# Optimization experiments

Hardware: AMD Instinct MI355X
Metric: run time of the kernel (lower is better)

Reference implementation:

```python
import jax, jax.numpy as jnp
import numpy as np

B, S, H = 2, 2048, 2048
NH, NKV, HD = 16, 4, 128
NEG = -1e9


def rotate_half(x):
    x1, x2 = x[..., : x.shape[-1] // 2], x[..., x.shape[-1] // 2 :]
    return jnp.concatenate((-x2, x1), axis=-1)


def setup_inputs() -> dict:
    key = jax.random.key(0)
    ks = jax.random.split(key, 6)
    hidden_states = jax.random.normal(ks[0], (B, S, H), dtype=jnp.float32)
    # causal additive mask [B, 1, S, S]
    causal = jnp.tril(jnp.ones((S, S), dtype=bool))
    attention_mask = jnp.where(causal, 0.0, NEG).astype(jnp.float32)
    attention_mask = jnp.broadcast_to(attention_mask, (B, 1, S, S))
    # rotary embeddings, base 10000
    inv_freq = 1.0 / (10000.0 ** (np.arange(0, HD, 2, dtype=np.float32) / HD))
    pos = np.arange(S, dtype=np.float32)
    freqs = np.outer(pos, inv_freq)  # [S, HD/2]
    emb = np.concatenate([freqs, freqs], axis=-1)  # [S, HD]
    cos = jnp.broadcast_to(jnp.asarray(np.cos(emb)), (B, S, HD))
    sin = jnp.broadcast_to(jnp.asarray(np.sin(emb)), (B, S, HD))
    sc = 0.02
    Wq = jax.random.normal(ks[1], (H, NH * HD), dtype=jnp.float32) * sc
    Wk = jax.random.normal(ks[2], (H, NKV * HD), dtype=jnp.float32) * sc
    Wv = jax.random.normal(ks[3], (H, NKV * HD), dtype=jnp.float32) * sc
    Wo = jax.random.normal(ks[4], (H, H), dtype=jnp.float32) * sc
    return {"hidden_states": hidden_states, "attention_mask": attention_mask,
            "cos": cos, "sin": sin, "Wq": Wq, "Wk": Wk, "Wv": Wv, "Wo": Wo}


def reference(hidden_states, attention_mask, cos, sin, Wq, Wk, Wv, Wo):
    b, s, _ = hidden_states.shape
    # projections -> [b, heads, s, hd]
    q = (hidden_states @ Wq).reshape(b, s, NH, HD).transpose(0, 2, 1, 3)
    k = (hidden_states @ Wk).reshape(b, s, NKV, HD).transpose(0, 2, 1, 3)
    v = (hidden_states @ Wv).reshape(b, s, NKV, HD).transpose(0, 2, 1, 3)
    # RoPE (cos/sin unsqueezed at dim 1)
    c, sn = cos[:, None], sin[:, None]
    q = q * c + rotate_half(q) * sn
    k = k * c + rotate_half(k) * sn
    # GQA repeat_kv: [b, nkv, s, hd] -> [b, nh, s, hd]
    n_rep = NH // NKV
    k = jnp.repeat(k, n_rep, axis=1)
    v = jnp.repeat(v, n_rep, axis=1)
    scores = jnp.einsum("bhqd,bhkd->bhqk", q, k) / jnp.sqrt(jnp.float32(HD))
    scores = scores + attention_mask
    probs = jax.nn.softmax(scores.astype(jnp.float32), axis=-1).astype(q.dtype)
    out = jnp.einsum("bhqk,bhkd->bhqd", probs, v)
    out = out.transpose(0, 2, 1, 3).reshape(b, s, NH * HD)
    return out @ Wo
```

## Files before the change

kernel.cpp:

```cpp
#include <hip/hip_runtime.h>
#include <hip/hip_bf16.h>

typedef __bf16 bf16;
typedef __bf16 bf16x4 __attribute__((ext_vector_type(4)));
typedef __bf16 bf16x8 __attribute__((ext_vector_type(8)));
typedef float f32x4 __attribute__((ext_vector_type(4)));

__device__ __forceinline__ void gload_lds16(const void* g, void* l) {
  __builtin_amdgcn_global_load_lds((__attribute__((address_space(1))) void*)(g),
                                   (__attribute__((address_space(3))) void*)(l), 16, 0, 0);
}
__device__ __forceinline__ float fexp2(float x) {
  float r;
  asm volatile("v_exp_f32 %0, %1" : "=v"(r) : "v"(x));
  return r;
}
#define S_WAITCNT_VM(n) asm volatile("s_waitcnt vmcnt(" #n ")" ::: "memory")
#define LDS_FENCE() asm volatile("" ::: "memory")

__global__ void k_diag(float* __restrict__ o, float v) { o[threadIdx.x] = v; }

__global__ void k_cvt_bf16(const float* __restrict__ x, bf16* __restrict__ y, int n4) {
  int i = blockIdx.x * blockDim.x + threadIdx.x;
  if (i < n4) {
    float4 v = reinterpret_cast<const float4*>(x)[i];
    bf16x4 o = {(bf16)v.x, (bf16)v.y, (bf16)v.z, (bf16)v.w};
    reinterpret_cast<bf16x4*>(y)[i] = o;
  }
}

__global__ void k_transpose_w(const float* __restrict__ W, bf16* __restrict__ Wt, int K, int N) {
  __shared__ float tile[32][33];
  int kb = blockIdx.x * 32, nb = blockIdx.y * 32;
  int tx = threadIdx.x & 31, ty = threadIdx.x >> 5;
#pragma unroll
  for (int i = 0; i < 32; i += 8)
    tile[ty + i][tx] = W[(size_t)(kb + ty + i) * N + nb + tx];
  __syncthreads();
#pragma unroll
  for (int i = 0; i < 32; i += 8)
    Wt[(size_t)(nb + ty + i) * K + kb + tx] = (bf16)tile[tx][ty + i];
}

__global__ void k_transpose_v(const bf16* __restrict__ Cq, bf16* __restrict__ Vt) {
  __shared__ bf16 tile[32][34];
  constexpr int S = 2048, CSTR = 3072;
  int sb = blockIdx.x * 32, db = blockIdx.y * 32, bh = blockIdx.z;
  int b = bh >> 2, kvh = bh & 3;
  int tx = threadIdx.x & 31, ty = threadIdx.x >> 5;
  const bf16* src = Cq + (size_t)b * S * CSTR + 2560 + kvh * 128;
#pragma unroll
  for (int i = 0; i < 32; i += 8)
    tile[ty + i][tx] = src[(size_t)(sb + ty + i) * CSTR + db + tx];
  __syncthreads();
  bf16* dst = Vt + (size_t)bh * 128 * S;
#pragma unroll
  for (int i = 0; i < 32; i += 8)
    dst[(size_t)(db + ty + i) * S + sb + tx] = tile[tx][ty + i];
}

template <typename OT>
__global__ __launch_bounds__(512) void k_gemm4(const bf16* __restrict__ A,
                                               const bf16* __restrict__ B0,
                                               const bf16* __restrict__ B1, int nsplit,
                                               OT* __restrict__ C, int Ncols, int Kd) {
  __shared__ __align__(16) char lds[131072];
  const int t = threadIdx.x, w = t >> 6, l = t & 63;
  const int lr = l & 15, lk = l >> 4;
  const int gx = gridDim.x;
  const int flat = blockIdx.y * gx + blockIdx.x;
  const int xcd = flat & 7, local = flat >> 3;
  const int mi = (xcd & 3) * (gx >> 2) + (local & ((gx >> 2) - 1));
  const int ni = (xcd >> 2) * (gridDim.y >> 1) + (local >> 2);
  const int m0 = mi * 256, n0 = ni * 256;
  const int wm = w >> 2, wn = w & 3;
  const bf16* Bt = (n0 < nsplit) ? B0 + (size_t)n0 * Kd : B1 + (size_t)(n0 - nsplit) * Kd;
  const int nkt = Kd >> 6;
  const int srow8 = l >> 3;
  const int sk = ((l & 7) ^ srow8) * 8;
  auto stA = [&](int kt, int g) {
    if (kt >= nkt) return;
    const bf16* s = A + (size_t)(m0 + w * 32 + g * 8 + srow8) * Kd + (kt << 6) + sk;
    gload_lds16(s, lds + (kt & 1) * 32768 + (w * 32 + g * 8) * 128);
  };
  auto stB = [&](int kt, int g) {
    if (kt >= nkt) return;
    const bf16* s = Bt + (size_t)(w * 32 + g * 8 + srow8) * Kd + (kt << 6) + sk;
    gload_lds16(s, lds + 65536 + (kt & 1) * 32768 + (w * 32 + g * 8) * 128);
  };

  f32x4 acc[8][4] = {};
#pragma unroll
  for (int g = 0; g < 4; ++g) { stA(0, g); stB(0, g); }

  for (int kt = 0; kt < nkt; ++kt) {
    const char* Ab = lds + (kt & 1) * 32768;
    const char* Bb = lds + 65536 + (kt & 1) * 32768;
    bf16x8 bfr[4];
#pragma unroll
    for (int kk = 0; kk < 2; ++kk) {
#pragma unroll
      for (int h = 0; h < 2; ++h) {
        if (kk == 0 && h == 0) { S_WAITCNT_VM(0); }
        __builtin_amdgcn_s_barrier();
        LDS_FENCE();
        const int ph = kk * 2 + h;
        stA(kt + 1, ph);
        stB(kt + 1, ph);
        const int rc = ((kk * 4 + lk) ^ (lr & 7)) << 4;
        bf16x8 af[4];
#pragma unroll
        for (int i = 0; i < 4; ++i)
          af[i] = *reinterpret_cast<const bf16x8*>(Ab + (wm * 128 + (h * 4 + i) * 16 + lr) * 128 + rc);
        if (h == 0) {
#pragma unroll
          for (int j = 0; j < 4; ++j)
            bfr[j] = *reinterpret_cast<const bf16x8*>(Bb + (wn * 64 + j * 16 + lr) * 128 + rc);
        }
        __builtin_amdgcn_s_setprio(1);
#pragma unroll
        for (int i = 0; i < 4; ++i)
#pragma unroll
          for (int j = 0; j < 4; ++j)
            acc[h * 4 + i][j] = __builtin_amdgcn_mfma_f32_16x16x32_bf16(af[i], bfr[j], acc[h * 4 + i][j], 0, 0, 0);
        __builtin_amdgcn_s_setprio(0);
      }
    }
  }
#pragma unroll
  for (int i = 0; i < 8; ++i)
#pragma unroll
    for (int j = 0; j < 4; ++j)
#pragma unroll
      for (int r = 0; r < 4; ++r) {
        int row = m0 + wm * 128 + i * 16 + lk * 4 + r;
        int col = n0 + wn * 64 + j * 16 + lr;
        if constexpr (sizeof(OT) == 4)
          C[(size_t)row * Ncols + col] = acc[i][j][r];
        else
          C[(size_t)row * Ncols + col] = (bf16)acc[i][j][r];
      }
}

template <int BM, typename OT>
__global__ __launch_bounds__(512) void k_gemm2(const bf16* __restrict__ A, const bf16* __restrict__ Bt,
                                               OT* __restrict__ C, int N, int Kd) {
  constexpr int NA = (BM / 16) * 2;
  constexpr int NB = 16;
  constexpr int NST = NA + NB;
  constexpr int NSW = NST / 8;
  constexpr int WM = BM / 4;
  constexpr int RG = WM / 16;
  __shared__ __align__(16) bf16 sAB[2][NST * 512];
  const int t = threadIdx.x, w = t >> 6, l = t & 63;
  const int lr = l & 15, lk = l >> 4;
  const int gx = gridDim.x;
  const int nwg = gx * gridDim.y;
  const int flat = blockIdx.y * gx + blockIdx.x;
  const int vid = (flat & 7) * (nwg >> 3) + (flat >> 3);
  const int m0 = (vid % gx) * BM, n0 = (vid / gx) * 128;
  const int wm = w >> 1, wn = w & 1;
  const int srow = l >> 2;
  const int lchunk = (l & 3) ^ (((l >> 5) & 1) << 1);
  const int rdoff = lr * 64 + ((lk * 16) ^ ((lr >> 3) << 5));
  const int nkt = Kd >> 6;
  char* lds = (char*)sAB;

  auto stage = [&](int kt, int buf) {
    const int k0 = kt << 6;
#pragma unroll
    for (int u = 0; u < NSW; ++u) {
      const int s = w * NSW + u;
      const bf16* src;
      if (s < NA)
        src = A + (size_t)(m0 + (s >> 1) * 16 + srow) * Kd + k0 + (s & 1) * 32 + lchunk * 8;
      else
        src = Bt + (size_t)(n0 + ((s - NA) >> 1) * 16 + srow) * Kd + k0 + ((s - NA) & 1) * 32 + lchunk * 8;
      gload_lds16(src, lds + buf * (NST * 1024) + s * 1024);
    }
  };

  f32x4 acc[RG][4] = {};
  stage(0, 0);
  stage(1, 1);
  if constexpr (NSW == 6) S_WAITCNT_VM(6); else S_WAITCNT_VM(4);
  __builtin_amdgcn_s_barrier();
  int c = 0;
  for (int kt = 0; kt < nkt; ++kt) {
    __builtin_amdgcn_sched_barrier(0);
    const char* base = lds + c * (NST * 1024);
    bf16x8 af[RG][2], bfr[4][2];
#pragma unroll
    for (int i = 0; i < RG; ++i)
#pragma unroll
      for (int kk = 0; kk < 2; ++kk)
        af[i][kk] = *reinterpret_cast<const bf16x8*>(base + ((wm * RG + i) * 2 + kk) * 1024 + rdoff);
#pragma unroll
    for (int j = 0; j < 4; ++j)
#pragma unroll
      for (int kk = 0; kk < 2; ++kk)
        bfr[j][kk] = *reinterpret_cast<const bf16x8*>(base + (NA + (wn * 4 + j) * 2 + kk) * 1024 + rdoff);
    __builtin_amdgcn_s_setprio(1);
#pragma unroll
    for (int i = 0; i < RG; ++i)
#pragma unroll
      for (int j = 0; j < 4; ++j) {
        acc[i][j] = __builtin_amdgcn_mfma_f32_16x16x32_bf16(af[i][0], bfr[j][0], acc[i][j], 0, 0, 0);
        acc[i][j] = __builtin_amdgcn_mfma_f32_16x16x32_bf16(af[i][1], bfr[j][1], acc[i][j], 0, 0, 0);
      }
    __builtin_amdgcn_s_setprio(0);
    __builtin_amdgcn_sched_barrier(0);
    asm volatile("" ::: "memory");
    __builtin_amdgcn_s_barrier();
    if (kt + 2 < nkt) stage(kt + 2, c);
    if (kt + 1 < nkt) {
      if (kt + 2 < nkt) {
        if constexpr (NSW == 6) S_WAITCNT_VM(6); else S_WAITCNT_VM(4);
      } else {
        S_WAITCNT_VM(0);
      }
      asm volatile("" ::: "memory");
      __builtin_amdgcn_s_barrier();
    }
    c ^= 1;
  }
#pragma unroll
  for (int i = 0; i < RG; ++i)
#pragma unroll
    for (int j = 0; j < 4; ++j)
#pragma unroll
      for (int r = 0; r < 4; ++r) {
        int row = m0 + wm * WM + i * 16 + lk * 4 + r;
        int col = n0 + wn * 64 + j * 16 + lr;
        if constexpr (sizeof(OT) == 4)
          C[(size_t)row * N + col] = acc[i][j][r];
        else
          C[(size_t)row * N + col] = (bf16)acc[i][j][r];
      }
}

__global__ void k_rope(bf16* __restrict__ X, const float* __restrict__ cs, const float* __restrict__ sn,
                       int nh, int rowstride, float scale, int total) {
  int idx = blockIdx.x * blockDim.x + threadIdx.x;
  if (idx >= total) return;
  int d = idx & 63;
  int th = idx >> 6;
  int h = th % nh;
  int tok = th / nh;
  size_t base = (size_t)tok * rowstride + h * 128;
  float c = cs[tok * 128 + d], s = sn[tok * 128 + d];
  float x1 = (float)X[base + d];
  float x2 = (float)X[base + d + 64];
  X[base + d] = (bf16)((x1 * c - x2 * s) * scale);
  X[base + d + 64] = (bf16)((x2 * c + x1 * s) * scale);
}

__global__ __launch_bounds__(512) void k_attn(const bf16* __restrict__ Q, const bf16* __restrict__ KV,
                                              const bf16* __restrict__ Vt, bf16* __restrict__ O) {
  constexpr int S = 2048, HD = 128, QSTR = 3072, OSTR = 2048;
  __shared__ __align__(16) char smem[81920];
  const int bid = blockIdx.x;
  const int vid = (bid & 7) * 32 + (bid >> 3);
  const int p = vid & 7, bh = vid >> 3;
  const int h = bh & 15, b = bh >> 4;
  const int t = threadIdx.x, w = t >> 6, l = t & 63;
  const int wq = w & 3, wk = w >> 2;
  const int lr = l & 15, lk = l >> 4;
  const int kvh = h >> 2;
  const int swz = (lr & 7) << 4;

  const char* kbase = (const char*)(KV + (size_t)b * S * QSTR + kvh * HD);
  const int krow_l = w * 8 + (l >> 4);
  const int kcol_l = (l & 15) << 4;
  const char* vtbase = (const char*)(Vt + (size_t)(b * 4 + kvh) * HD * S);
  const int vrow_l = w * 16 + (l >> 3);
  const int vcol_l = (l & 7) << 4;
  auto stage = [&](int kvb, int buf) {
#pragma unroll
    for (int c = 0; c < 2; ++c) {
      const int krow = krow_l + c * 4;
      gload_lds16(kbase + (size_t)(kvb + krow) * (QSTR * 2) + (kcol_l ^ ((krow & 7) << 4)),
                  smem + buf * 16384 + (w * 2 + c) * 1024);
      const int vrow = vrow_l + c * 8;
      gload_lds16(vtbase + (size_t)vrow * (S * 2) + kvb * 2 + (vcol_l ^ ((vrow & 7) << 4)),
                  smem + 32768 + buf * 16384 + (w * 2 + c) * 1024);
    }
  };
  char* sPb = smem + 65536 + w * 1280;

  for (int seg = 0; seg < 2; ++seg) {
    const int qtl = seg ? (15 - p) : p;
    const int qw = qtl * 128 + wq * 32;
    const int qlast = qw + 31;
    const int ntiles = (qtl + 1) * 2;
    int cur = 0;
    __syncthreads();
    stage(0, 0);
    bf16x8 qf[2][4];
#pragma unroll
    for (int rg = 0; rg < 2; ++rg) {
      const bf16* Qp = Q + (size_t)(b * S + qw + rg * 16 + lr) * QSTR + h * HD + lk * 8;
#pragma unroll
      for (int i = 0; i < 4; ++i) qf[rg][i] = *reinterpret_cast<const bf16x8*>(Qp + i * 32);
    }
    f32x4 oacc[2][8] = {};
    float mrow[2][4] = {{-1e30f, -1e30f, -1e30f, -1e30f}, {-1e30f, -1e30f, -1e30f, -1e30f}};
    float lsum[2][4] = {};
    __syncthreads();
    for (int tt = 0; tt < ntiles; ++tt) {
      const int kvb = tt * 64;
      if (tt + 1 < ntiles) stage(kvb + 64, cur ^ 1);
      const char* sKc = smem + cur * 16384;
      const char* sVc = smem + 32768 + cur * 16384;
      const int col0 = kvb + wk * 32;
      if (col0 <= qlast) {
        float pm[2][2][4];
#pragma unroll
        for (int c = 0; c < 2; ++c) {
          f32x4 s0 = {}, s1 = {};
#pragma unroll
          for (int kf = 0; kf < 4; ++kf) {
            bf16x8 kf8 = *reinterpret_cast<const bf16x8*>(
                sKc + (wk * 32 + c * 16 + lr) * 256 + (((kf * 64) + (lk << 4)) ^ swz));
            s0 = __builtin_amdgcn_mfma_f32_16x16x32_bf16(qf[0][kf], kf8, s0, 0, 0, 0);
            s1 = __builtin_amdgcn_mfma_f32_16x16x32_bf16(qf[1][kf], kf8, s1, 0, 0, 0);
          }
#pragma unroll
          for (int r = 0; r < 4; ++r) { pm[0][c][r] = s0[r]; pm[1][c][r] = s1[r]; }
        }
        if (col0 + 31 > qw) {
#pragma unroll
          for (int rg = 0; rg < 2; ++rg)
#pragma unroll
            for (int c = 0; c < 2; ++c) {
              const int col = col0 + c * 16 + lr;
#pragma unroll
              for (int r = 0; r < 4; ++r)
                if (col > qw + rg * 16 + lk * 4 + r) pm[rg][c][r] = -1e38f;
            }
        }
        float pmax[2][4];
#pragma unroll
        for (int rg = 0; rg < 2; ++rg)
#pragma unroll
          for (int r = 0; r < 4; ++r) pmax[rg][r] = fmaxf(pm[rg][0][r], pm[rg][1][r]);
        bool hi = false;
#pragma unroll
        for (int rg = 0; rg < 2; ++rg)
#pragma unroll
          for (int r = 0; r < 4; ++r) hi |= (pmax[rg][r] > mrow[rg][r] + 8.f);
        if (__any(hi)) {
          float mx[2][4];
#pragma unroll
          for (int rg = 0; rg < 2; ++rg)
#pragma unroll
            for (int r = 0; r < 4; ++r) mx[rg][r] = pmax[rg][r];
#pragma unroll
          for (int off = 1; off < 16; off <<= 1)
#pragma unroll
            for (int rg = 0; rg < 2; ++rg)
#pragma unroll
              for (int r = 0; r < 4; ++r) mx[rg][r] = fmaxf(mx[rg][r], __shfl_xor(mx[rg][r], off));
#pragma unroll
          for (int rg = 0; rg < 2; ++rg)
#pragma unroll
            for (int r = 0; r < 4; ++r) {
              float mn = fmaxf(mrow[rg][r], mx[rg][r]);
              float fac = fexp2(mrow[rg][r] - mn);
              mrow[rg][r] = mn;
              lsum[rg][r] *= fac;
#pragma unroll
              for (int ch = 0; ch < 8; ++ch) oacc[rg][ch][r] *= fac;
            }
        }
#pragma unroll
        for (int rg = 0; rg < 2; ++rg) {
#pragma unroll
          for (int c = 0; c < 2; ++c)
#pragma unroll
            for (int r = 0; r < 4; ++r) pm[rg][c][r] = fexp2(pm[rg][c][r] - mrow[rg][r]);
#pragma unroll
          for (int r = 0; r < 4; ++r) lsum[rg][r] += pm[rg][0][r] + pm[rg][1][r];
        }
        bf16x8 pf[2];
#pragma unroll
        for (int rg = 0; rg < 2; ++rg) {
#pragma unroll
          for (int c = 0; c < 2; ++c)
#pragma unroll
            for (int r = 0; r < 4; ++r)
              *(bf16*)(sPb + (lk * 4 + r) * 80 + (c * 16 + lr) * 2) = (bf16)pm[rg][c][r];
          pf[rg] = *reinterpret_cast<const bf16x8*>(sPb + lr * 80 + lk * 16);
        }
#pragma unroll
        for (int ch = 0; ch < 8; ++ch) {
          bf16x8 vf = *reinterpret_cast<const bf16x8*>(
              sVc + (ch * 16 + lr) * 128 + ((wk * 64 + (lk << 4)) ^ swz));
          oacc[0][ch] = __builtin_amdgcn_mfma_f32_16x16x32_bf16(pf[0], vf, oacc[0][ch], 0, 0, 0);
          oacc[1][ch] = __builtin_amdgcn_mfma_f32_16x16x32_bf16(pf[1], vf, oacc[1][ch], 0, 0, 0);
        }
      }
      __syncthreads();
      cur ^= 1;
    }
#pragma unroll
    for (int off = 1; off < 16; off <<= 1)
#pragma unroll
      for (int rg = 0; rg < 2; ++rg)
#pragma unroll
        for (int r = 0; r < 4; ++r) lsum[rg][r] += __shfl_xor(lsum[rg][r], off);
    float* ob = (float*)smem;
    float* mlb = (float*)(smem + 65536);
    if (wk == 1) {
#pragma unroll
      for (int rg = 0; rg < 2; ++rg) {
#pragma unroll
        for (int ch = 0; ch < 8; ++ch)
          *reinterpret_cast<f32x4*>(&ob[wq * 4096 + l * 64 + (rg * 8 + ch) * 4]) = oacc[rg][ch];
#pragma unroll
        for (int r = 0; r < 4; ++r) {
          mlb[wq * 1024 + l * 16 + rg * 8 + r] = mrow[rg][r];
          mlb[wq * 1024 + l * 16 + rg * 8 + 4 + r] = lsum[rg][r];
        }
      }
    }
    __syncthreads();
    if (wk == 0) {
      float sc0[2][4], sc1[2][4];
#pragma unroll
      for (int rg = 0; rg < 2; ++rg)
#pragma unroll
        for (int r = 0; r < 4; ++r) {
          float m1 = mlb[wq * 1024 + l * 16 + rg * 8 + r];
          float l1 = mlb[wq * 1024 + l * 16 + rg * 8 + 4 + r];
          float m = fmaxf(mrow[rg][r], m1);
          float w0 = fexp2(mrow[rg][r] - m), w1 = fexp2(m1 - m);
          float inv = 1.0f / (lsum[rg][r] * w0 + l1 * w1);
          sc0[rg][r] = w0 * inv;
          sc1[rg][r] = w1 * inv;
        }
#pragma unroll
      for (int rg = 0; rg < 2; ++rg) {
        bf16* Op = O + (size_t)(b * S + qw + rg * 16) * OSTR + h * HD;
#pragma unroll
        for (int ch = 0; ch < 8; ++ch) {
          f32x4 o1 = *reinterpret_cast<const f32x4*>(&ob[wq * 4096 + l * 64 + (rg * 8 + ch) * 4]);
#pragma unroll
          for (int r = 0; r < 4; ++r)
            Op[(size_t)(lk * 4 + r) * OSTR + ch * 16 + lr] =
                (bf16)(oacc[rg][ch][r] * sc0[rg][r] + o1[r] * sc1[rg][r]);
        }
      }
    }
  }
}

extern "C" void kernel_launch(void* const* d_in, const int* in_sizes, int n_in,
                              void* d_out, int out_size, void* d_ws, size_t ws_size,
                              hipStream_t stream) {
  const float* hs = (const float*)d_in[0];
  const float* cosb = (const float*)d_in[2];
  const float* sinb = (const float*)d_in[3];
  const float* Wq = (const float*)d_in[4];
  const float* Wk = (const float*)d_in[5];
  const float* Wv = (const float*)d_in[6];
  const float* Wo = (const float*)d_in[7];
  float* out = (float*)d_out;

  constexpr int B = 2, S = 2048, H = 2048, NH = 16, NKV = 4, HD = 128;
  constexpr int T = B * S;
  constexpr size_t MB = 1024 * 1024;

  const size_t ws_need = 24 * MB;
  if (ws_size < ws_need) {
    k_diag<<<1, 64, 0, stream>>>(out, 1000.0f + (float)(ws_size / MB));
    return;
  }
  bf16* Xb = (bf16*)d_ws;
  bf16* WtQ = (bf16*)((char*)d_ws + 16 * MB);
  bf16* Ob = Xb;
  bf16* Cqkv = (bf16*)d_out;
  bf16* Vtb = (bf16*)((char*)d_out + 24 * MB);
  bf16* WtKV = (bf16*)((char*)d_out + 28 * MB);

  k_cvt_bf16<<<T * H / 4 / 256, 256, 0, stream>>>(hs, Xb, T * H / 4);

  k_transpose_w<<<dim3(H / 32, H / 32), 256, 0, stream>>>(Wq, WtQ, H, H);
  k_transpose_w<<<dim3(H / 32, (NKV * HD) / 32), 256, 0, stream>>>(Wk, WtKV, H, NKV * HD);
  k_transpose_w<<<dim3(H / 32, (NKV * HD) / 32), 256, 0, stream>>>(Wv, WtKV + (size_t)(NKV * HD) * H, H, NKV * HD);

  k_gemm4<bf16><<<dim3(16, 12), 512, 0, stream>>>(Xb, WtQ, WtKV, 2048, Cqkv, 3072, H);

  k_transpose_v<<<dim3(S / 32, HD / 32, B * NKV), 256, 0, stream>>>(Cqkv, Vtb);

  const float qscale = 0.12751743f;
  k_rope<<<(T * NH * 64) / 256, 256, 0, stream>>>(Cqkv, cosb, sinb, NH, 3072, qscale, T * NH * 64);
  k_rope<<<(T * NKV * 64) / 256, 256, 0, stream>>>(Cqkv + 2048, cosb, sinb, NKV, 3072, 1.0f, T * NKV * 64);

  k_attn<<<256, 512, 0, stream>>>(Cqkv, Cqkv + 2048, Vtb, Ob);

  k_transpose_w<<<dim3(H / 32, H / 32), 256, 0, stream>>>(Wo, WtQ, H, H);
  k_gemm2<256, float><<<dim3(16, 16), 512, 0, stream>>>(Ob, WtQ, out, H, H);
}
```

Baseline: 213.3 us.

## Replace output-projection GEMM with 128x256 tile kernel using XOR-swizzled LDS

Replaces the output projection GEMM with a new kernel. It uses 128x256 tiles (previously 256x128), a 2x4 wave layout, 128-byte rows in LDS with an XOR swizzle, and global-to-LDS prefetch split across two k-substeps with a full vmcnt wait each iteration. It also changes the attention kernel's cross-wave partial-output staging in LDS to a lane-contiguous layout, aimed at reducing bank conflicts. The new GEMM's pipeline waits for all outstanding loads every iteration, which may expose memory latency compared with the earlier depth-two prefetch.

```diff
diff --git a/kernel.cpp b/kernel.cpp
--- a/kernel.cpp
+++ b/kernel.cpp
@@ -142,100 +142,73 @@
       }
 }
 
-template <int BM, typename OT>
-__global__ __launch_bounds__(512) void k_gemm2(const bf16* __restrict__ A, const bf16* __restrict__ Bt,
-                                               OT* __restrict__ C, int N, int Kd) {
-  constexpr int NA = (BM / 16) * 2;
-  constexpr int NB = 16;
-  constexpr int NST = NA + NB;
-  constexpr int NSW = NST / 8;
-  constexpr int WM = BM / 4;
-  constexpr int RG = WM / 16;
-  __shared__ __align__(16) bf16 sAB[2][NST * 512];
+template <typename OT>
+__global__ __launch_bounds__(512) void k_gemm5(const bf16* __restrict__ A, const bf16* __restrict__ Bt,
+                                               OT* __restrict__ C, int Ncols, int Kd) {
+  __shared__ __align__(16) char lds[98304];
   const int t = threadIdx.x, w = t >> 6, l = t & 63;
   const int lr = l & 15, lk = l >> 4;
   const int gx = gridDim.x;
-  const int nwg = gx * gridDim.y;
   const int flat = blockIdx.y * gx + blockIdx.x;
-  const int vid = (flat & 7) * (nwg >> 3) + (flat >> 3);
-  const int m0 = (vid % gx) * BM, n0 = (vid / gx) * 128;
-  const int wm = w >> 1, wn = w & 1;
-  const int srow = l >> 2;
-  const int lchunk = (l & 3) ^ (((l >> 5) & 1) << 1);
-  const int rdoff = lr * 64 + ((lk * 16) ^ ((lr >> 3) << 5));
+  const int vid = (flat & 7) * 32 + (flat >> 3);
+  const int m0 = (vid & 31) * 128, n0 = (vid >> 5) * 256;
+  const int wm = w >> 2, wn = w & 3;
   const int nkt = Kd >> 6;
-  char* lds = (char*)sAB;
-
-  auto stage = [&](int kt, int buf) {
-    const int k0 = kt << 6;
-#pragma unroll
-    for (int u = 0; u < NSW; ++u) {
-      const int s = w * NSW + u;
-      const bf16* src;
-      if (s < NA)
-        src = A + (size_t)(m0 + (s >> 1) * 16 + srow) * Kd + k0 + (s & 1) * 32 + lchunk * 8;
-      else
-        src = Bt + (size_t)(n0 + ((s - NA) >> 1) * 16 + srow) * Kd + k0 + ((s - NA) & 1) * 32 + lchunk * 8;
-      gload_lds16(src, lds + buf * (NST * 1024) + s * 1024);
-    }
+  const int srow8 = l >> 3;
+  const int sk = ((l & 7) ^ srow8) * 8;
+  auto stA = [&](int kt, int g) {
+    if (kt >= nkt) return;
+    const bf16* s = A + (size_t)(m0 + w * 16 + g * 8 + srow8) * Kd + (kt << 6) + sk;
+    gload_lds16(s, lds + (kt & 1) * 16384 + (w * 16 + g * 8) * 128);
   };
-
-  f32x4 acc[RG][4] = {};
-  stage(0, 0);
-  stage(1, 1);
-  if constexpr (NSW == 6) S_WAITCNT_VM(6); else S_WAITCNT_VM(4);
-  __builtin_amdgcn_s_barrier();
-  int c = 0;
+  auto stB = [&](int kt, int g) {
+    if (kt >= nkt) return;
+    const bf16* s = Bt + (size_t)(n0 + w * 32 + g * 8 + srow8) * Kd + (kt << 6) + sk;
+    gload_lds16(s, lds + 32768 + (kt & 1) * 32768 + (w * 32 + g * 8) * 128);
+  };
+
+  f32x4 acc[4][4] = {};
+  stA(0, 0); stA(0, 1); stB(0, 0); stB(0, 1); stB(0, 2); stB(0, 3);
+
   for (int kt = 0; kt < nkt; ++kt) {
-    __builtin_amdgcn_sched_barrier(0);
-    const char* base = lds + c * (NST * 1024);
-    bf16x8 af[RG][2], bfr[4][2];
-#pragma unroll
-    for (int i = 0; i < RG; ++i)
-#pragma unroll
-      for (int kk = 0; kk < 2; ++kk)
-        af[i][kk] = *reinterpret_cast<const bf16x8*>(base + ((wm * RG + i) * 2 + kk) * 1024 + rdoff);
+    const char* Ab = lds + (kt & 1) * 16384;
+    const char* Bb = lds + 32768 + (kt & 1) * 32768;
+#pragma unroll
+    for (int kk = 0; kk < 2; ++kk) {
+      if (kk == 0) { S_WAITCNT_VM(0); }
+      __builtin_amdgcn_s_barrier();
+      LDS_FENCE();
+      if (kk == 0) { stA(kt + 1, 0); stA(kt + 1, 1); stB(kt + 1, 0); }
+      else { stB(kt + 1, 1); stB(kt + 1, 2); stB(kt + 1, 3); }
+      const int rc = ((kk * 4 + lk) ^ (lr & 7)) << 4;
+      bf16x8 af[4], bfr[4];
+#pragma unroll
+      for (int i = 0; i < 4; ++i)
+        af[i] = *reinterpret_cast<const bf16x8*>(Ab + (wm * 64 + i * 16 + lr) * 128 + rc);
+#pragma unroll
+      for (int j = 0; j < 4; ++j)
+        bfr[j] = *reinterpret_cast<const bf16x8*>(Bb + (wn * 64 + j * 16 + lr) * 128 + rc);
+      __builtin_amdgcn_s_setprio(1);
+#pragma unroll
+      for (int i = 0; i < 4; ++i)
+#pragma unroll
+        for (int j = 0; j < 4; ++j)
+          acc[i][j] = __builtin_amdgcn_mfma_f32_16x16x32_bf16(af[i], bfr[j], acc[i][j], 0, 0, 0);
+      __builtin_amdgcn_s_setprio(0);
+    }
+  }
+#pragma unroll
+  for (int i = 0; i < 4; ++i)
 #pragma unroll
     for (int j = 0; j < 4; ++j)
 #pragma unroll
-      for (int kk = 0; kk < 2; ++kk)
-        bfr[j][kk] = *reinterpret_cast<const bf16x8*>(base + (NA + (wn * 4 + j) * 2 + kk) * 1024 + rdoff);
-    __builtin_amdgcn_s_setprio(1);
-#pragma unroll
-    for (int i = 0; i < RG; ++i)
-#pragma unroll
-      for (int j = 0; j < 4; ++j) {
-        acc[i][j] = __builtin_amdgcn_mfma_f32_16x16x32_bf16(af[i][0], bfr[j][0], acc[i][j], 0, 0, 0);
-        acc[i][j] = __builtin_amdgcn_mfma_f32_16x16x32_bf16(af[i][1], bfr[j][1], acc[i][j], 0, 0, 0);
-      }
-    __builtin_amdgcn_s_setprio(0);
-    __builtin_amdgcn_sched_barrier(0);
-    asm volatile("" ::: "memory");
-    __builtin_amdgcn_s_barrier();
-    if (kt + 2 < nkt) stage(kt + 2, c);
-    if (kt + 1 < nkt) {
-      if (kt + 2 < nkt) {
-        if constexpr (NSW == 6) S_WAITCNT_VM(6); else S_WAITCNT_VM(4);
-      } else {
-        S_WAITCNT_VM(0);
-      }
-      asm volatile("" ::: "memory");
-      __builtin_amdgcn_s_barrier();
-    }
-    c ^= 1;
-  }
-#pragma unroll
-  for (int i = 0; i < RG; ++i)
-#pragma unroll
-    for (int j = 0; j < 4; ++j)
-#pragma unroll
       for (int r = 0; r < 4; ++r) {
-        int row = m0 + wm * WM + i * 16 + lk * 4 + r;
+        int row = m0 + wm * 64 + i * 16 + lk * 4 + r;
         int col = n0 + wn * 64 + j * 16 + lr;
         if constexpr (sizeof(OT) == 4)
-          C[(size_t)row * N + col] = acc[i][j][r];
+          C[(size_t)row * Ncols + col] = acc[i][j][r];
         else
-          C[(size_t)row * N + col] = (bf16)acc[i][j][r];
+          C[(size_t)row * Ncols + col] = (bf16)acc[i][j][r];
       }
 }
 
@@ -416,7 +389,7 @@
       for (int rg = 0; rg < 2; ++rg) {
 #pragma unroll
         for (int ch = 0; ch < 8; ++ch)
-          *reinterpret_cast<f32x4*>(&ob[wq * 4096 + l * 64 + (rg * 8 + ch) * 4]) = oacc[rg][ch];
+          *reinterpret_cast<f32x4*>(&ob[wq * 4096 + (rg * 8 + ch) * 256 + l * 4]) = oacc[rg][ch];
 #pragma unroll
         for (int r = 0; r < 4; ++r) {
           mlb[wq * 1024 + l * 16 + rg * 8 + r] = mrow[rg][r];
@@ -444,7 +417,7 @@
         bf16* Op = O + (size_t)(b * S + qw + rg * 16) * OSTR + h * HD;
 #pragma unroll
         for (int ch = 0; ch < 8; ++ch) {
-          f32x4 o1 = *reinterpret_cast<const f32x4*>(&ob[wq * 4096 + l * 64 + (rg * 8 + ch) * 4]);
+          f32x4 o1 = *reinterpret_cast<const f32x4*>(&ob[wq * 4096 + (rg * 8 + ch) * 256 + l * 4]);
 #pragma unroll
           for (int r = 0; r < 4; ++r)
             Op[(size_t)(lk * 4 + r) * OSTR + ch * 16 + lr] =
@@ -500,5 +473,5 @@
   k_attn<<<256, 512, 0, stream>>>(Cqkv, Cqkv + 2048, Vtb, Ob);
 
   k_transpose_w<<<dim3(H / 32, H / 32), 256, 0, stream>>>(Wo, WtQ, H, H);
-  k_gemm2<256, float><<<dim3(16, 16), 512, 0, stream>>>(Ob, WtQ, out, H, H);
-}
+  k_gemm5<float><<<dim3(32, 8), 512, 0, stream>>>(Ob, WtQ, out, H, H);
+}
```

New measurement: 210.2 us. No clear change (-1.5%).
